# Optimization experiments

Measured on AMD Instinct MI355X. Metric: run time of the kernel, lower is better.

## Reference

```python
import jax, jax.numpy as jnp
import numpy as np

B, C, H, W = 4, 128, 96, 96
INTER = C // 2


def setup_inputs() -> dict:
    key = jax.random.key(0)
    ks = jax.random.split(key, 6)
    scale = 1.0 / np.sqrt(C)
    return {
        "x1": jax.random.normal(ks[0], (B, C, H, W), dtype=jnp.float32),
        "x2": jax.random.normal(ks[1], (B, C, H, W), dtype=jnp.float32),
        "w_theta": jax.random.normal(ks[2], (INTER, C), dtype=jnp.float32) * scale,
        "w_phi": jax.random.normal(ks[3], (INTER, C), dtype=jnp.float32) * scale,
        "w_g": jax.random.normal(ks[4], (INTER, C), dtype=jnp.float32) * scale,
        "w_mask": jax.random.normal(ks[5], (C, INTER), dtype=jnp.float32) * (1.0 / np.sqrt(INTER)),
    }


def reference(x1, x2, w_theta, w_phi, w_g, w_mask):
    b, c, h1, w1 = x1.shape  # c == full channel
    inter = c // 2
    # 1x1 convs (no bias) == channel GEMMs
    theta = jnp.einsum('ic,bchw->bihw', w_theta, x1)   # [b, inter, h1, w1]
    phi   = jnp.einsum('ic,bchw->bihw', w_phi,   x2)   # [b, inter, h2, w2]
    g     = jnp.einsum('ic,bchw->bihw', w_g,     x2)   # [b, inter, h2, w2]
    # Faithful to original: .view(b, c, -1) with c = FULL channel count,
    # so the flattened length is H*W/2 and the contraction dim is c (row-major reshape).
    theta = theta.reshape(b, c, -1).transpose(0, 2, 1)  # [b, N1, c], N1 = h1*w1//2
    phi = phi.reshape(b, c, -1)                         # [b, c, N2]
    g = g.reshape(b, c, -1).transpose(0, 2, 1)          # [b, N2, c]
    scores = jnp.einsum('bnc,bcm->bnm', theta, phi)     # [b, N1, N2]
    attn = jax.nn.softmax(scores, axis=1)               # softmax over dim=1 (query axis!)
    y = jnp.einsum('bnm,bmc->bnc', attn, g)             # [b, N1, c]
    y = y.transpose(0, 2, 1).reshape(b, inter, h1, w1)  # [b, inter, h1, w1]
    mask = jnp.einsum('ci,bihw->bchw', w_mask, y)       # [b, c, h1, w1]
    return mask + x1
```

## Files before the change

### kernel.cpp

```cpp
#include <hip/hip_runtime.h>

typedef __attribute__((ext_vector_type(8))) short short8;
typedef __attribute__((ext_vector_type(4))) float f32x4;
typedef __attribute__((ext_vector_type(16))) float f32x16;
typedef unsigned short u16;
typedef unsigned int u32;

#define NB 4
#define CH 128
#define INTER2 64
#define HW2 9216
#define NN 4608
#define NSLICE 16
#define SLW2 288
#define SK 8
#define PCH 136
#define EPITCH 264

__device__ __forceinline__ u16 f2bf(float f) {
  u32 u = __float_as_uint(f);
  u += 0x7fffu + ((u >> 16) & 1u);
  return (u16)(u >> 16);
}
__device__ __forceinline__ float bf2f(u16 h) { return __uint_as_float(((u32)h) << 16); }
__device__ __forceinline__ u32 cvtpk(float lo, float hi) {
  u32 r;
  asm("v_cvt_pk_bf16_f32 %0, %1, %2" : "=v"(r) : "v"(lo), "v"(hi));
  return r;
}
__device__ __forceinline__ void gl_lds16(const u16* g, u16* l) {
  __builtin_amdgcn_global_load_lds(
      (const __attribute__((address_space(1))) unsigned int*)g,
      (__attribute__((address_space(3))) unsigned int*)l, 16, 0, 0);
}

__global__ void k_wcvt(const float* __restrict__ wt, const float* __restrict__ wp,
                       const float* __restrict__ wg, const float* __restrict__ wm,
                       u16* __restrict__ wtb, u16* __restrict__ wpb,
                       u16* __restrict__ wgb, u16* __restrict__ wmb) {
  int i = blockIdx.x * 256 + threadIdx.x;
  if (i < CH * INTER2) {
    wtb[i] = f2bf(wt[i]);
    wpb[i] = f2bf(wp[i]);
    wgb[i] = f2bf(wg[i]);
    wmb[i] = f2bf(wm[i]);
  }
}

__global__ __launch_bounds__(256) void k_conv(const float* __restrict__ x1,
                                              const float* __restrict__ x2,
                                              const u16* __restrict__ wtb,
                                              const u16* __restrict__ wpb,
                                              const u16* __restrict__ wgb,
                                              u16* __restrict__ Tt,
                                              u16* __restrict__ Pt,
                                              u16* __restrict__ Gn) {
  __shared__ u16 xT[64 * PCH];
  __shared__ u16 ot[64 * 72];
  const int tid = threadIdx.x;
  const int w = tid >> 6, l = tid & 63, lr = l & 15, lg = l >> 4;
  const int pt = blockIdx.x, b = blockIdx.y, z = blockIdx.z;
  const int p0 = pt * 64;
  const int h = (p0 >= NN) ? 1 : 0;
  const int n0 = p0 - h * NN;
  const float* X = (z ? x2 : x1) + (size_t)b * CH * HW2;

  {
    const int pq = (l & 15) * 4;
    const int cs = w + 4 * (l >> 4);
#pragma unroll
    for (int it = 0; it < 8; it++) {
      const int c = it * 16 + cs;
      float4 v = *(const float4*)(X + (size_t)c * HW2 + p0 + pq);
      xT[(pq + 0) * PCH + c] = f2bf(v.x);
      xT[(pq + 1) * PCH + c] = f2bf(v.y);
      xT[(pq + 2) * PCH + c] = f2bf(v.z);
      xT[(pq + 3) * PCH + c] = f2bf(v.w);
    }
  }
  short8 wsP[4], wsG[4];
  {
    const u16* W1 = z ? wpb : wtb;
#pragma unroll
    for (int ks = 0; ks < 4; ks++)
      wsP[ks] = *(const short8*)(W1 + (w * 16 + lr) * CH + ks * 32 + lg * 8);
    if (z) {
#pragma unroll
      for (int ks = 0; ks < 4; ks++)
        wsG[ks] = *(const short8*)(wgb + (w * 16 + lr) * CH + ks * 32 + lg * 8);
    }
  }
  __syncthreads();
  short8 xf[4][4];
#pragma unroll
  for (int tp = 0; tp < 4; tp++)
#pragma unroll
    for (int ks = 0; ks < 4; ks++)
      xf[tp][ks] = *(const short8*)(&xT[(tp * 16 + lr) * PCH + ks * 32 + lg * 8]);

  f32x4 accP[4];
#pragma unroll
  for (int tp = 0; tp < 4; tp++) {
#pragma unroll
    for (int j = 0; j < 4; j++) accP[tp][j] = 0.f;
#pragma unroll
    for (int ks = 0; ks < 4; ks++)
      accP[tp] = __builtin_amdgcn_mfma_f32_16x16x32_bf16(xf[tp][ks], wsP[ks], accP[tp], 0, 0, 0);
  }
#pragma unroll
  for (int tp = 0; tp < 4; tp++) {
#pragma unroll
    for (int j = 0; j < 4; j++)
      ot[(tp * 16 + lg * 4 + j) * 72 + w * 16 + lr] = f2bf(accP[tp][j]);
  }
  if (z) {
    f32x4 accG[4];
#pragma unroll
    for (int tp = 0; tp < 4; tp++) {
#pragma unroll
      for (int j = 0; j < 4; j++) accG[tp][j] = 0.f;
#pragma unroll
      for (int ks = 0; ks < 4; ks++)
        accG[tp] = __builtin_amdgcn_mfma_f32_16x16x32_bf16(wsG[ks], xf[tp][ks], accG[tp], 0, 0, 0);
    }
    u16* Gb = Gn + (size_t)b * CH * NN;
#pragma unroll
    for (int tp = 0; tp < 4; tp++) {
#pragma unroll
      for (int j = 0; j < 4; j++) {
        const int ig = w * 16 + lg * 4 + j;
        Gb[(size_t)((h << 6) + ig) * NN + n0 + tp * 16 + lr] = f2bf(accG[tp][j]);
      }
    }
  }
  __syncthreads();
  {
    u16* dst = (z ? Pt : Tt) + (size_t)b * NN * CH;
#pragma unroll
    for (int q = 0; q < 2; q++) {
      const int idx = tid * 2 + q;
      const int p = idx >> 3, c8 = (idx & 7) * 8;
      uint4 v = *(const uint4*)(&ot[p * 72 + c8]);
      *(uint4*)(dst + (size_t)(n0 + p) * CH + h * 64 + c8) = v;
    }
  }
}

__global__ __launch_bounds__(256) void k_scores(const u16* __restrict__ Tt,
                                                const u16* __restrict__ Pt,
                                                u16* __restrict__ E,
                                                float* __restrict__ denp,
                                                int b0) {
  __shared__ u16 Et[32 * EPITCH];
  const int tid = threadIdx.x;
  const int w = tid >> 6, l = tid & 63, lm = l & 31, lh = l >> 5;
  const int s = blockIdx.x & 15, mt = blockIdx.x >> 4;
  const int eb = blockIdx.y, b = b0 + eb;
  const int m0 = mt * 256;
  const int nbase = s * SLW2;
  const u16* PtB = Pt + (size_t)b * NN * CH;
  const u16* TtB = Tt + (size_t)b * NN * CH;
  u16* Eb = E + (size_t)eb * NN * NN;

  short8 bf[2][8];
#pragma unroll
  for (int ms = 0; ms < 2; ms++)
#pragma unroll
    for (int ks = 0; ks < 8; ks++)
      bf[ms][ks] = *(const short8*)(PtB + (size_t)(m0 + w * 64 + ms * 32 + lm) * CH + ks * 16 + lh * 8);

  float den0 = 0.f, den1 = 0.f;
  short8 ac[8], an[8];
#pragma unroll
  for (int ks = 0; ks < 8; ks++)
    ac[ks] = *(const short8*)(TtB + (size_t)(nbase + lm) * CH + ks * 16 + lh * 8);

  for (int it = 0; it < 9; it++) {
    if (it + 1 < 9) {
      const int nr = nbase + (it + 1) * 32 + lm;
#pragma unroll
      for (int ks = 0; ks < 8; ks++)
        an[ks] = *(const short8*)(TtB + (size_t)nr * CH + ks * 16 + lh * 8);
    }
    f32x16 a0, a1;
#pragma unroll
    for (int q = 0; q < 16; q++) { a0[q] = 0.f; a1[q] = 0.f; }
#pragma unroll
    for (int ks = 0; ks < 8; ks++) {
      a0 = __builtin_amdgcn_mfma_f32_32x32x16_bf16(ac[ks], bf[0][ks], a0, 0, 0, 0);
      a1 = __builtin_amdgcn_mfma_f32_32x32x16_bf16(ac[ks], bf[1][ks], a1, 0, 0, 0);
    }
#pragma unroll
    for (int q = 0; q < 16; q++) {
      const int nl = (q & 3) + 8 * (q >> 2) + 4 * lh;
      float e0 = exp2f(__builtin_fmaf(a0[q], 1.44269504f, -57.70780163f));
      float e1 = exp2f(__builtin_fmaf(a1[q], 1.44269504f, -57.70780163f));
      den0 += e0;
      den1 += e1;
      Et[nl * EPITCH + w * 64 + lm] = f2bf(e0);
      Et[nl * EPITCH + w * 64 + 32 + lm] = f2bf(e1);
    }
    __syncthreads();
    {
      const int r = tid >> 3, cq = tid & 7;
      const int ng = nbase + it * 32 + r;
      u16* dst = Eb + (size_t)ng * NN + m0;
#pragma unroll
      for (int k = 0; k < 4; k++) {
        const int col = k * 64 + cq * 8;
        *(uint4*)(dst + col) = *(const uint4*)(&Et[r * EPITCH + col]);
      }
    }
    __syncthreads();
    if (it + 1 < 9) {
#pragma unroll
      for (int ks = 0; ks < 8; ks++) ac[ks] = an[ks];
    }
  }
  den0 += __shfl_xor(den0, 32, 64);
  den1 += __shfl_xor(den1, 32, 64);
  if (l < 32) {
    float* dp = denp + (size_t)(s * NB + b) * NN + m0 + w * 64;
    dp[lm] = den0;
    dp[32 + lm] = den1;
  }
}

__global__ __launch_bounds__(256) void k_gd(const u16* __restrict__ Gn,
                                            const float* __restrict__ denp,
                                            u16* __restrict__ Gd,
                                            int b0) {
  const int q = blockIdx.x * 256 + threadIdx.x;
  const int d = q / 576, mc = q % 576;
  const int m0 = mc * 8;
  const int b = b0 + blockIdx.y;
  float dn[8];
#pragma unroll
  for (int i = 0; i < 8; i++) dn[i] = 0.f;
#pragma unroll
  for (int s = 0; s < NSLICE; s++) {
    const float* dp = denp + (size_t)(s * NB + b) * NN + m0;
    float4 a = *(const float4*)dp;
    float4 c = *(const float4*)(dp + 4);
    dn[0] += a.x; dn[1] += a.y; dn[2] += a.z; dn[3] += a.w;
    dn[4] += c.x; dn[5] += c.y; dn[6] += c.z; dn[7] += c.w;
  }
  const size_t off = (size_t)b * CH * NN + (size_t)d * NN + m0;
  uint4 v = *(const uint4*)(Gn + off);
  u32 arr[4] = {v.x, v.y, v.z, v.w};
  uint4 o;
  u32 ov[4];
#pragma unroll
  for (int j = 0; j < 4; j++) {
    float lo = bf2f((u16)(arr[j] & 0xffffu)) / dn[2 * j];
    float hi = bf2f((u16)(arr[j] >> 16)) / dn[2 * j + 1];
    ov[j] = cvtpk(lo, hi);
  }
  o.x = ov[0]; o.y = ov[1]; o.z = ov[2]; o.w = ov[3];
  *(uint4*)(Gd + off) = o;
}

__global__ __launch_bounds__(256) void k_pv(const u16* __restrict__ E,
                                            const u16* __restrict__ Gd,
                                            float* __restrict__ Yp,
                                            int b0) {
  __shared__ u16 lA[128 * 64];
  __shared__ u16 lB[128 * 64];
  const int tid = threadIdx.x;
  const int w = tid >> 6, l = tid & 63, lr = l & 15, lg = l >> 4;
  const int sk = blockIdx.x / 36, nt = blockIdx.x % 36;
  const int eb = blockIdx.y, b = b0 + eb;
  const int n0 = nt * 128;
  const int k0 = sk * (NN / SK);
  const u16* Eb = E + (size_t)eb * NN * NN;
  const u16* Gb = Gd + (size_t)b * CH * NN;
  const int wm = w >> 1, wn2 = w & 1;
  const int rl = l >> 3;
  const int cg = (l & 7) ^ rl;

  f32x4 acc[4][4];
#pragma unroll
  for (int fa = 0; fa < 4; fa++)
#pragma unroll
    for (int fb = 0; fb < 4; fb++)
#pragma unroll
      for (int j = 0; j < 4; j++) acc[fa][fb][j] = 0.f;

#define STAGE(kk)                                                                   \
  {                                                                                 \
    _Pragma("unroll") for (int r = 0; r < 4; r++) {                                 \
      const int rowA = r * 32 + w * 8 + rl;                                         \
      gl_lds16(Gb + (size_t)rowA * NN + (kk) + cg * 8, &lA[(r * 32 + w * 8) * 64]); \
      gl_lds16(Eb + (size_t)(n0 + rowA) * NN + (kk) + cg * 8,                       \
               &lB[(r * 32 + w * 8) * 64]);                                         \
    }                                                                               \
  }

  STAGE(k0);
  const int NKS = (NN / SK) / 64;
  for (int st = 0; st < NKS; st++) {
    __syncthreads();
#pragma unroll
    for (int ks2 = 0; ks2 < 2; ks2++) {
      const int cw = ((ks2 * 4 + lg) ^ (lr & 7)) * 8;
      short8 af[4], bfr[4];
#pragma unroll
      for (int fa = 0; fa < 4; fa++)
        af[fa] = *(const short8*)(&lA[(wm * 64 + fa * 16 + lr) * 64 + cw]);
#pragma unroll
      for (int fb = 0; fb < 4; fb++)
        bfr[fb] = *(const short8*)(&lB[(wn2 * 64 + fb * 16 + lr) * 64 + cw]);
#pragma unroll
      for (int fa = 0; fa < 4; fa++)
#pragma unroll
        for (int fb = 0; fb < 4; fb++)
          acc[fa][fb] = __builtin_amdgcn_mfma_f32_16x16x32_bf16(af[fa], bfr[fb], acc[fa][fb], 0, 0, 0);
    }
    __syncthreads();
    if (st + 1 < NKS) STAGE(k0 + (st + 1) * 64);
  }
#undef STAGE
  const int slab = sk * 2 + eb;
  float* Yb = Yp + (size_t)slab * CH * NN;
#pragma unroll
  for (int fa = 0; fa < 4; fa++) {
#pragma unroll
    for (int fb = 0; fb < 4; fb++) {
      const int n = n0 + wn2 * 64 + fb * 16 + lr;
#pragma unroll
      for (int j = 0; j < 4; j++) {
        const int cc = wm * 64 + fa * 16 + lg * 4 + j;
        Yb[(size_t)cc * NN + n] = acc[fa][fb][j];
      }
    }
  }
}

__global__ __launch_bounds__(256) void k_out(const float* __restrict__ Yp,
                                             const u16* __restrict__ wmb,
                                             const float* __restrict__ x1,
                                             float* __restrict__ out,
                                             int b0) {
  __shared__ u16 yy[64][72];
  const int tid = threadIdx.x;
  const int w = tid >> 6, l = tid & 63, lr = l & 15, lg = l >> 4;
  const int eb = blockIdx.y, b = b0 + eb;
  const int n0 = blockIdx.x * 32;
  const int nl = tid & 31, cch = tid >> 5;

  float v[16];
#pragma unroll
  for (int q = 0; q < 16; q++) v[q] = 0.f;
  for (int s2 = 0; s2 < SK; s2++) {
    const float* base = Yp + ((size_t)(s2 * 2 + eb) * CH + cch * 16) * NN + n0 + nl;
#pragma unroll
    for (int q = 0; q < 16; q++) v[q] += base[(size_t)q * NN];
  }
#pragma unroll
  for (int q = 0; q < 16; q++) {
    const int d = cch * 16 + q;
    yy[(d >> 6) * 32 + nl][d & 63] = f2bf(v[q]);
  }
  __syncthreads();

  const int wm3 = w >> 1, wp3 = w & 1;
  f32x4 eacc[4][2];
#pragma unroll
  for (int fa = 0; fa < 4; fa++)
#pragma unroll
    for (int fb = 0; fb < 2; fb++)
#pragma unroll
      for (int j = 0; j < 4; j++) eacc[fa][fb][j] = 0.f;
#pragma unroll
  for (int ks = 0; ks < 2; ks++) {
    short8 wa[4];
#pragma unroll
    for (int fa = 0; fa < 4; fa++)
      wa[fa] = *(const short8*)(wmb + (wm3 * 64 + fa * 16 + lr) * 64 + ks * 32 + lg * 8);
    short8 yb[2];
#pragma unroll
    for (int fb = 0; fb < 2; fb++)
      yb[fb] = *(const short8*)(&yy[wp3 * 32 + fb * 16 + lr][ks * 32 + lg * 8]);
#pragma unroll
    for (int fa = 0; fa < 4; fa++)
#pragma unroll
      for (int fb = 0; fb < 2; fb++)
        eacc[fa][fb] = __builtin_amdgcn_mfma_f32_16x16x32_bf16(wa[fa], yb[fb], eacc[fa][fb], 0, 0, 0);
  }
  const float* x1b = x1 + (size_t)b * CH * HW2;
  float* ob = out + (size_t)b * CH * HW2;
#pragma unroll
  for (int fa = 0; fa < 4; fa++) {
#pragma unroll
    for (int fb = 0; fb < 2; fb++) {
      const int pl = wp3 * 32 + fb * 16 + lr;
      const int col = n0 + (pl & 31) + (pl >> 5) * NN;
#pragma unroll
      for (int j = 0; j < 4; j++) {
        const int c = wm3 * 64 + fa * 16 + lg * 4 + j;
        const size_t o = (size_t)c * HW2 + col;
        ob[o] = eacc[fa][fb][j] + x1b[o];
      }
    }
  }
}

extern "C" void kernel_launch(void* const* d_in, const int* in_sizes, int n_in,
                              void* d_out, int out_size, void* d_ws, size_t ws_size,
                              hipStream_t stream) {
  const float* x1 = (const float*)d_in[0];
  const float* x2 = (const float*)d_in[1];
  const float* wt = (const float*)d_in[2];
  const float* wp = (const float*)d_in[3];
  const float* wg = (const float*)d_in[4];
  const float* wm = (const float*)d_in[5];
  float* out = (float*)d_out;

  char* ws = (char*)d_ws;
  const size_t SZ_T = (size_t)NB * NN * CH * 2;
  u16* Tt = (u16*)ws; ws += SZ_T;
  u16* Pt = (u16*)ws; ws += SZ_T;
  u16* Gn = (u16*)ws; ws += SZ_T;
  u16* Gd = (u16*)ws; ws += SZ_T;
  float* denp = (float*)ws; ws += (size_t)NSLICE * NB * NN * 4;
  u16* wtb = (u16*)ws; ws += (size_t)CH * INTER2 * 2;
  u16* wpb = (u16*)ws; ws += (size_t)CH * INTER2 * 2;
  u16* wgb = (u16*)ws; ws += (size_t)CH * INTER2 * 2;
  u16* wmb = (u16*)ws; ws += (size_t)CH * INTER2 * 2;
  float* Yp = (float*)ws; ws += (size_t)16 * CH * NN * 4;
  u16* E = (u16*)ws;

  const size_t fixed = (size_t)(ws - (char*)d_ws);
  const size_t eslab = (size_t)NN * NN * 2;
  int eslots = 0;
  if (ws_size >= fixed + 2 * eslab) eslots = 2;
  else if (ws_size >= fixed + 1 * eslab) eslots = 1;
  if (eslots == 0) return;

  hipLaunchKernelGGL(k_wcvt, dim3(32), dim3(256), 0, stream, wt, wp, wg, wm, wtb, wpb, wgb, wmb);
  hipLaunchKernelGGL(k_conv, dim3(144, NB, 2), dim3(256), 0, stream, x1, x2, wtb, wpb, wgb, Tt, Pt, Gn);
  for (int b0 = 0; b0 < NB; b0 += eslots) {
    hipLaunchKernelGGL(k_scores, dim3(18 * 16, eslots), dim3(256), 0, stream, Tt, Pt, E, denp, b0);
    hipLaunchKernelGGL(k_gd, dim3(288, eslots), dim3(256), 0, stream, Gn, denp, Gd, b0);
    hipLaunchKernelGGL(k_pv, dim3(SK * 36, eslots), dim3(256), 0, stream, E, Gd, Yp, b0);
    hipLaunchKernelGGL(k_out, dim3(144, eslots), dim3(256), 0, stream, Yp, wmb, x1, out, b0);
  }
}
```

Baseline: 208.7 us.

## Fuse score recomputation with PV GEMM to avoid materializing the attention matrix

Drops the stored bf16 exp-score matrix E (NN×NN per batch) and its normalization pass. A first kernel computes only the softmax column denominators, a small kernel turns them into reciprocals, and a fused attention kernel recomputes the scores per tile, scales them by the reciprocal and feeds them straight into the PV MFMA through LDS. This removes roughly 170MB of E write and read traffic and the batch-sliced launch loop. In exchange the QK^T GEMM is done twice and the G fragments are now read directly from global memory.

```diff
diff --git a/kernel.cpp b/kernel.cpp
--- a/kernel.cpp
+++ b/kernel.cpp
@@ -13,9 +13,8 @@
 #define NN 4608
 #define NSLICE 16
 #define SLW2 288
-#define SK 8
 #define PCH 136
-#define EPITCH 264
+#define APITCH 136
 
 __device__ __forceinline__ u16 f2bf(float f) {
   u32 u = __float_as_uint(f);
@@ -146,21 +145,17 @@
   }
 }
 
-__global__ __launch_bounds__(256) void k_scores(const u16* __restrict__ Tt,
-                                                const u16* __restrict__ Pt,
-                                                u16* __restrict__ E,
-                                                float* __restrict__ denp,
-                                                int b0) {
-  __shared__ u16 Et[32 * EPITCH];
+__global__ __launch_bounds__(256) void k_den(const u16* __restrict__ Tt,
+                                             const u16* __restrict__ Pt,
+                                             float* __restrict__ denp) {
   const int tid = threadIdx.x;
   const int w = tid >> 6, l = tid & 63, lm = l & 31, lh = l >> 5;
   const int s = blockIdx.x & 15, mt = blockIdx.x >> 4;
-  const int eb = blockIdx.y, b = b0 + eb;
+  const int b = blockIdx.y;
   const int m0 = mt * 256;
   const int nbase = s * SLW2;
   const u16* PtB = Pt + (size_t)b * NN * CH;
   const u16* TtB = Tt + (size_t)b * NN * CH;
-  u16* Eb = E + (size_t)eb * NN * NN;
 
   short8 bf[2][8];
 #pragma unroll
@@ -192,26 +187,9 @@
     }
 #pragma unroll
     for (int q = 0; q < 16; q++) {
-      const int nl = (q & 3) + 8 * (q >> 2) + 4 * lh;
-      float e0 = exp2f(__builtin_fmaf(a0[q], 1.44269504f, -57.70780163f));
-      float e1 = exp2f(__builtin_fmaf(a1[q], 1.44269504f, -57.70780163f));
-      den0 += e0;
-      den1 += e1;
-      Et[nl * EPITCH + w * 64 + lm] = f2bf(e0);
-      Et[nl * EPITCH + w * 64 + 32 + lm] = f2bf(e1);
-    }
-    __syncthreads();
-    {
-      const int r = tid >> 3, cq = tid & 7;
-      const int ng = nbase + it * 32 + r;
-      u16* dst = Eb + (size_t)ng * NN + m0;
-#pragma unroll
-      for (int k = 0; k < 4; k++) {
-        const int col = k * 64 + cq * 8;
-        *(uint4*)(dst + col) = *(const uint4*)(&Et[r * EPITCH + col]);
-      }
-    }
-    __syncthreads();
+      den0 += exp2f(__builtin_fmaf(a0[q], 1.44269504f, -57.70780163f));
+      den1 += exp2f(__builtin_fmaf(a1[q], 1.44269504f, -57.70780163f));
+    }
     if (it + 1 < 9) {
 #pragma unroll
       for (int ks = 0; ks < 8; ks++) ac[ks] = an[ks];
@@ -226,58 +204,48 @@
   }
 }
 
-__global__ __launch_bounds__(256) void k_gd(const u16* __restrict__ Gn,
-                                            const float* __restrict__ denp,
-                                            u16* __restrict__ Gd,
-                                            int b0) {
-  const int q = blockIdx.x * 256 + threadIdx.x;
-  const int d = q / 576, mc = q % 576;
-  const int m0 = mc * 8;
-  const int b = b0 + blockIdx.y;
-  float dn[8];
-#pragma unroll
-  for (int i = 0; i < 8; i++) dn[i] = 0.f;
-#pragma unroll
-  for (int s = 0; s < NSLICE; s++) {
-    const float* dp = denp + (size_t)(s * NB + b) * NN + m0;
-    float4 a = *(const float4*)dp;
-    float4 c = *(const float4*)(dp + 4);
-    dn[0] += a.x; dn[1] += a.y; dn[2] += a.z; dn[3] += a.w;
-    dn[4] += c.x; dn[5] += c.y; dn[6] += c.z; dn[7] += c.w;
-  }
-  const size_t off = (size_t)b * CH * NN + (size_t)d * NN + m0;
-  uint4 v = *(const uint4*)(Gn + off);
-  u32 arr[4] = {v.x, v.y, v.z, v.w};
-  uint4 o;
-  u32 ov[4];
-#pragma unroll
-  for (int j = 0; j < 4; j++) {
-    float lo = bf2f((u16)(arr[j] & 0xffffu)) / dn[2 * j];
-    float hi = bf2f((u16)(arr[j] >> 16)) / dn[2 * j + 1];
-    ov[j] = cvtpk(lo, hi);
-  }
-  o.x = ov[0]; o.y = ov[1]; o.z = ov[2]; o.w = ov[3];
-  *(uint4*)(Gd + off) = o;
-}
-
-__global__ __launch_bounds__(256) void k_pv(const u16* __restrict__ E,
-                                            const u16* __restrict__ Gd,
-                                            float* __restrict__ Yp,
-                                            int b0) {
-  __shared__ u16 lA[128 * 64];
-  __shared__ u16 lB[128 * 64];
+__global__ __launch_bounds__(256) void k_rdn(const float* __restrict__ denp,
+                                             float* __restrict__ rdn) {
+  const int i = blockIdx.x * 256 + threadIdx.x;
+  const int b = i / NN, m = i % NN;
+  float s = 0.f;
+#pragma unroll
+  for (int s2 = 0; s2 < NSLICE; s2++) s += denp[(size_t)(s2 * NB + b) * NN + m];
+  rdn[i] = 1.0f / s;
+}
+
+__global__ __launch_bounds__(256) void k_att(const u16* __restrict__ Tt,
+                                             const u16* __restrict__ Pt,
+                                             const u16* __restrict__ Gn,
+                                             const float* __restrict__ rdn,
+                                             float* __restrict__ Yp) {
+  __shared__ u16 TtS[128 * 128];
+  __shared__ u16 Atile[128 * APITCH];
   const int tid = threadIdx.x;
   const int w = tid >> 6, l = tid & 63, lr = l & 15, lg = l >> 4;
-  const int sk = blockIdx.x / 36, nt = blockIdx.x % 36;
-  const int eb = blockIdx.y, b = b0 + eb;
+  const int lm = l & 31, lh = l >> 5;
+  const int x = blockIdx.x;
+  const int xcd = x & 7, rr = x >> 3;
+  const int nt = rr >> 1;
+  const int c = xcd + 8 * (rr & 1);
+  const int b = c >> 2, sk = c & 3;
   const int n0 = nt * 128;
-  const int k0 = sk * (NN / SK);
-  const u16* Eb = E + (size_t)eb * NN * NN;
-  const u16* Gb = Gd + (size_t)b * CH * NN;
-  const int wm = w >> 1, wn2 = w & 1;
-  const int rl = l >> 3;
-  const int cg = (l & 7) ^ rl;
-
+  const int mbase = sk * 1152;
+  const u16* TtB = Tt + ((size_t)b * NN + n0) * CH;
+  const u16* PtB = Pt + (size_t)b * NN * CH;
+  const u16* GnB = Gn + (size_t)b * CH * NN;
+  const float* rdnB = rdn + b * NN;
+
+#pragma unroll
+  for (int it = 0; it < 8; it++) {
+    const int i = it * 256 + tid;
+    const int row = i >> 4, slot = i & 15;
+    gl_lds16(TtB + (size_t)row * CH + ((slot ^ (row & 15)) * 8),
+             &TtS[(it * 256 + w * 64) * 8]);
+  }
+  __syncthreads();
+
+  const int wc = w >> 1, wn = w & 1;
   f32x4 acc[4][4];
 #pragma unroll
   for (int fa = 0; fa < 4; fa++)
@@ -286,51 +254,63 @@
 #pragma unroll
       for (int j = 0; j < 4; j++) acc[fa][fb][j] = 0.f;
 
-#define STAGE(kk)                                                                   \
-  {                                                                                 \
-    _Pragma("unroll") for (int r = 0; r < 4; r++) {                                 \
-      const int rowA = r * 32 + w * 8 + rl;                                         \
-      gl_lds16(Gb + (size_t)rowA * NN + (kk) + cg * 8, &lA[(r * 32 + w * 8) * 64]); \
-      gl_lds16(Eb + (size_t)(n0 + rowA) * NN + (kk) + cg * 8,                       \
-               &lB[(r * 32 + w * 8) * 64]);                                         \
-    }                                                                               \
-  }
-
-  STAGE(k0);
-  const int NKS = (NN / SK) / 64;
-  for (int st = 0; st < NKS; st++) {
+  for (int ch = 0; ch < 9; ch++) {
+    const int mch = mbase + ch * 128;
+    short8 bf[8];
+#pragma unroll
+    for (int ks = 0; ks < 8; ks++)
+      bf[ks] = *(const short8*)(PtB + (size_t)(mch + w * 32 + lm) * CH + ks * 16 + lh * 8);
+    const float rv = rdnB[mch + w * 32 + lm];
+#pragma unroll
+    for (int ns = 0; ns < 4; ns++) {
+      short8 af[8];
+#pragma unroll
+      for (int ks = 0; ks < 8; ks++)
+        af[ks] = *(const short8*)(&TtS[(ns * 32 + lm) * 128 + (((ks * 2 + lh) ^ (lm & 15)) * 8)]);
+      f32x16 sa;
+#pragma unroll
+      for (int q = 0; q < 16; q++) sa[q] = 0.f;
+#pragma unroll
+      for (int ks = 0; ks < 8; ks++)
+        sa = __builtin_amdgcn_mfma_f32_32x32x16_bf16(af[ks], bf[ks], sa, 0, 0, 0);
+#pragma unroll
+      for (int q = 0; q < 16; q += 2) {
+        const int nl = ns * 32 + (q & 3) + 8 * (q >> 2) + 4 * lh;
+        float e0 = exp2f(__builtin_fmaf(sa[q], 1.44269504f, -57.70780163f)) * rv;
+        float e1 = exp2f(__builtin_fmaf(sa[q + 1], 1.44269504f, -57.70780163f)) * rv;
+        u32 pk = cvtpk(e0, e1);
+        Atile[nl * APITCH + w * 32 + lm] = (u16)pk;
+        Atile[(nl + 1) * APITCH + w * 32 + lm] = (u16)(pk >> 16);
+      }
+    }
     __syncthreads();
 #pragma unroll
-    for (int ks2 = 0; ks2 < 2; ks2++) {
-      const int cw = ((ks2 * 4 + lg) ^ (lr & 7)) * 8;
-      short8 af[4], bfr[4];
+    for (int ks = 0; ks < 4; ks++) {
+      short8 gf[4], pb[4];
 #pragma unroll
       for (int fa = 0; fa < 4; fa++)
-        af[fa] = *(const short8*)(&lA[(wm * 64 + fa * 16 + lr) * 64 + cw]);
+        gf[fa] = *(const short8*)(GnB + (size_t)(wc * 64 + fa * 16 + lr) * NN + mch + ks * 32 + lg * 8);
 #pragma unroll
       for (int fb = 0; fb < 4; fb++)
-        bfr[fb] = *(const short8*)(&lB[(wn2 * 64 + fb * 16 + lr) * 64 + cw]);
+        pb[fb] = *(const short8*)(&Atile[(wn * 64 + fb * 16 + lr) * APITCH + ks * 32 + lg * 8]);
 #pragma unroll
       for (int fa = 0; fa < 4; fa++)
 #pragma unroll
         for (int fb = 0; fb < 4; fb++)
-          acc[fa][fb] = __builtin_amdgcn_mfma_f32_16x16x32_bf16(af[fa], bfr[fb], acc[fa][fb], 0, 0, 0);
+          acc[fa][fb] = __builtin_amdgcn_mfma_f32_16x16x32_bf16(gf[fa], pb[fb], acc[fa][fb], 0, 0, 0);
     }
     __syncthreads();
-    if (st + 1 < NKS) STAGE(k0 + (st + 1) * 64);
-  }
-#undef STAGE
-  const int slab = sk * 2 + eb;
-  float* Yb = Yp + (size_t)slab * CH * NN;
+  }
+  float* Yb = Yp + (size_t)(sk * NB + b) * CH * NN;
 #pragma unroll
   for (int fa = 0; fa < 4; fa++) {
 #pragma unroll
     for (int fb = 0; fb < 4; fb++) {
-      const int n = n0 + wn2 * 64 + fb * 16 + lr;
+      const int n = n0 + wn * 64 + fb * 16 + lr;
 #pragma unroll
       for (int j = 0; j < 4; j++) {
-        const int cc = wm * 64 + fa * 16 + lg * 4 + j;
-        Yb[(size_t)cc * NN + n] = acc[fa][fb][j];
+        const int d = wc * 64 + fa * 16 + lg * 4 + j;
+        Yb[(size_t)d * NN + n] = acc[fa][fb][j];
       }
     }
   }
@@ -339,20 +319,20 @@
 __global__ __launch_bounds__(256) void k_out(const float* __restrict__ Yp,
                                              const u16* __restrict__ wmb,
                                              const float* __restrict__ x1,
-                                             float* __restrict__ out,
-                                             int b0) {
+                                             float* __restrict__ out) {
   __shared__ u16 yy[64][72];
   const int tid = threadIdx.x;
   const int w = tid >> 6, l = tid & 63, lr = l & 15, lg = l >> 4;
-  const int eb = blockIdx.y, b = b0 + eb;
+  const int b = blockIdx.y;
   const int n0 = blockIdx.x * 32;
   const int nl = tid & 31, cch = tid >> 5;
 
   float v[16];
 #pragma unroll
   for (int q = 0; q < 16; q++) v[q] = 0.f;
-  for (int s2 = 0; s2 < SK; s2++) {
-    const float* base = Yp + ((size_t)(s2 * 2 + eb) * CH + cch * 16) * NN + n0 + nl;
+#pragma unroll
+  for (int s2 = 0; s2 < 4; s2++) {
+    const float* base = Yp + ((size_t)(s2 * NB + b) * CH + cch * 16) * NN + n0 + nl;
 #pragma unroll
     for (int q = 0; q < 16; q++) v[q] += base[(size_t)q * NN];
   }
@@ -421,28 +401,19 @@
   u16* Tt = (u16*)ws; ws += SZ_T;
   u16* Pt = (u16*)ws; ws += SZ_T;
   u16* Gn = (u16*)ws; ws += SZ_T;
-  u16* Gd = (u16*)ws; ws += SZ_T;
   float* denp = (float*)ws; ws += (size_t)NSLICE * NB * NN * 4;
+  float* rdn = (float*)ws; ws += (size_t)NB * NN * 4;
   u16* wtb = (u16*)ws; ws += (size_t)CH * INTER2 * 2;
   u16* wpb = (u16*)ws; ws += (size_t)CH * INTER2 * 2;
   u16* wgb = (u16*)ws; ws += (size_t)CH * INTER2 * 2;
   u16* wmb = (u16*)ws; ws += (size_t)CH * INTER2 * 2;
   float* Yp = (float*)ws; ws += (size_t)16 * CH * NN * 4;
-  u16* E = (u16*)ws;
-
-  const size_t fixed = (size_t)(ws - (char*)d_ws);
-  const size_t eslab = (size_t)NN * NN * 2;
-  int eslots = 0;
-  if (ws_size >= fixed + 2 * eslab) eslots = 2;
-  else if (ws_size >= fixed + 1 * eslab) eslots = 1;
-  if (eslots == 0) return;
+  if (ws_size < (size_t)(ws - (char*)d_ws)) return;
 
   hipLaunchKernelGGL(k_wcvt, dim3(32), dim3(256), 0, stream, wt, wp, wg, wm, wtb, wpb, wgb, wmb);
   hipLaunchKernelGGL(k_conv, dim3(144, NB, 2), dim3(256), 0, stream, x1, x2, wtb, wpb, wgb, Tt, Pt, Gn);
-  for (int b0 = 0; b0 < NB; b0 += eslots) {
-    hipLaunchKernelGGL(k_scores, dim3(18 * 16, eslots), dim3(256), 0, stream, Tt, Pt, E, denp, b0);
-    hipLaunchKernelGGL(k_gd, dim3(288, eslots), dim3(256), 0, stream, Gn, denp, Gd, b0);
-    hipLaunchKernelGGL(k_pv, dim3(SK * 36, eslots), dim3(256), 0, stream, E, Gd, Yp, b0);
-    hipLaunchKernelGGL(k_out, dim3(144, eslots), dim3(256), 0, stream, Yp, wmb, x1, out, b0);
-  }
-}
+  hipLaunchKernelGGL(k_den, dim3(288, NB), dim3(256), 0, stream, Tt, Pt, denp);
+  hipLaunchKernelGGL(k_rdn, dim3(72), dim3(256), 0, stream, denp, rdn);
+  hipLaunchKernelGGL(k_att, dim3(576), dim3(256), 0, stream, Tt, Pt, Gn, rdn, Yp);
+  hipLaunchKernelGGL(k_out, dim3(144, NB), dim3(256), 0, stream, Yp, wmb, x1, out);
+}
```

Result: faster. 198.5 us (-4.9%).
